# Kernel optimization log

Hardware: AMD Instinct MI355X
Metric: run time of the kernel (lower is better)

The kernel has to match this reference:

```python
import jax, jax.numpy as jnp
import numpy as np

B, T, C = 2, 2048, 1024
H = 16
D = C // H          # head_dim = 64
WIN = 256           # local window


def _rope(x):
    # x: [B, H, T, D]; rotate pairs (even, odd) with per-pair frequencies.
    t = x.shape[2]
    d = x.shape[-1] // 2
    theta = 10000.0 ** (-(jnp.arange(d, dtype=x.dtype) / d))          # [d]
    ang = jnp.arange(t, dtype=x.dtype)[:, None] * theta               # [T, d]
    sin, cos = jnp.sin(ang), jnp.cos(ang)                             # [T, d]
    x1, x2 = x[..., ::2], x[..., 1::2]                                # [B,H,T,d]
    out = jnp.stack([x1 * cos - x2 * sin, x1 * sin + x2 * cos], axis=-1)
    return out.reshape(x.shape)


def setup_inputs() -> dict:
    key = jax.random.key(0)
    k1, k2, k3 = jax.random.split(key, 3)
    s = 1.0 / np.sqrt(C)
    return {
        "x": jax.random.normal(k1, (B, T, C), dtype=jnp.float32),
        "w_qkv": jax.random.normal(k2, (3 * C, C), dtype=jnp.float32) * s,
        "w_out": jax.random.normal(k3, (C, C), dtype=jnp.float32) * s,
        "b_out": jnp.zeros((C,), dtype=jnp.float32),
    }


def reference(x, w_qkv, w_out, b_out):
    b, t, c = x.shape
    qkv = x @ w_qkv.T                                   # [B,T,3C]
    qkv = qkv.reshape(b, t, H, 3 * D).transpose(0, 2, 1, 3)  # [B,H,T,3D]
    q, k, v = jnp.split(qkv, 3, axis=-1)                # each [B,H,T,D]
    q, k = _rope(q), _rope(k)
    scores = jnp.einsum("bhqd,bhkd->bhqk", q, k) / jnp.sqrt(jnp.asarray(D, x.dtype))
    i = jnp.arange(t)[:, None]
    j = jnp.arange(t)[None, :]
    mask = (j <= i) & (j >= i - WIN)                    # causal local window
    scores = jnp.where(mask, scores, -jnp.inf)
    attn = jax.nn.softmax(scores, axis=-1)              # [B,H,T,T]
    out = jnp.einsum("bhqk,bhkd->bhqd", attn, v)        # [B,H,T,D]
    out = out.transpose(0, 2, 1, 3).reshape(b, t, c)    # [B,T,C]
    return out @ w_out.T + b_out
```

## Files before the change

kernel.cpp:

```cpp
#include <hip/hip_runtime.h>
#include <math.h>

#define BB 2
#define TT 2048
#define CC 1024
#define HH 16
#define DD 64
#define WINW 256

constexpr int MROWS  = BB * TT;
constexpr int NQKV   = 3 * CC;
constexpr int QKV_LD = 3 * CC;

typedef unsigned short ushort_t;
typedef __attribute__((ext_vector_type(8))) short  bf16x8;
typedef __attribute__((ext_vector_type(4))) float  f32x4;
typedef __attribute__((ext_vector_type(8))) unsigned short u16x8;

__device__ __forceinline__ float bf2f(ushort_t u) {
    return __uint_as_float(((unsigned int)u) << 16);
}
__device__ __forceinline__ ushort_t f2bf(float f) {
    unsigned int u = __float_as_uint(f);
    u += 0x7fffu + ((u >> 16) & 1u);
    return (ushort_t)(u >> 16);
}

__device__ __forceinline__ void async16(void* lds, const void* g) {
    __builtin_amdgcn_global_load_lds(
        (const __attribute__((address_space(1))) unsigned int*)g,
        (__attribute__((address_space(3))) unsigned int*)lds, 16, 0, 0);
}

#define ROPE_LN 0.2878231366242557f

constexpr int NX = MROWS * CC;
constexpr int NQ = NQKV * CC;
constexpr int NO = CC * CC;

__global__ __launch_bounds__(256)
void convert_all(const float* __restrict__ x, const float* __restrict__ wq,
                 const float* __restrict__ wo, ushort_t* __restrict__ xb,
                 ushort_t* __restrict__ wqb, ushort_t* __restrict__ wob) {
    int i = (blockIdx.x * 256 + threadIdx.x) * 4;
    const float* src;
    ushort_t* dst;
    if (i < NX)           { src = x  + i;             dst = xb  + i; }
    else if (i < NX + NQ) { src = wq + (i - NX);      dst = wqb + (i - NX); }
    else                  { src = wo + (i - NX - NQ); dst = wob + (i - NX - NQ); }
    float4 v = *(const float4*)src;
    ushort4 o;
    o.x = f2bf(v.x); o.y = f2bf(v.y); o.z = f2bf(v.z); o.w = f2bf(v.w);
    *(ushort4*)dst = o;
}

__global__ __launch_bounds__(512)
void gemm1_8phase(const ushort_t* __restrict__ A, const ushort_t* __restrict__ Bw,
                  ushort_t* __restrict__ Cc) {
    constexpr int K = 1024, N = 3072, NT = 16;
    __shared__ __align__(16) ushort_t As[2][2][256 * 32];
    __shared__ __align__(16) ushort_t Bs[2][2][256 * 32];

    const int tid  = threadIdx.x;
    const int lane = tid & 63;
    const int w    = tid >> 6;
    const int wm   = w >> 2;
    const int wn   = w & 3;
    const int fr   = lane & 15;
    const int fq   = lane >> 4;

    const int nbx = NQKV / 256;
    int flat = blockIdx.y * nbx + blockIdx.x;
    flat = (flat & 7) * 24 + (flat >> 3);
    const int bm = (flat / nbx) * 256;
    const int bn = (flat % nbx) * 256;

    const int sr  = tid >> 2;
    const int dcb = tid & 3;
    const int scb = dcb ^ ((sr >> 1) & 3);

    const int cbr = fq ^ ((fr >> 1) & 3);

    f32x4 acc[8][4];
#pragma unroll
    for (int m = 0; m < 8; ++m)
#pragma unroll
        for (int n = 0; n < 4; ++n)
            acc[m][n] = f32x4{0.f, 0.f, 0.f, 0.f};

#pragma unroll
    for (int p = 0; p < 4; ++p) {
        const int skh = p >> 1;
        const bool isB = p & 1;
        const ushort_t* G = isB ? Bw : A;
        const int br = isB ? bn : bm;
        ushort_t* L = isB ? &Bs[0][skh][0] : &As[0][skh][0];
#pragma unroll
        for (int hh = 0; hh < 2; ++hh)
            async16(&L[(hh * 128 + sr) * 32 + dcb * 8],
                    G + (size_t)(br + hh * 128 + sr) * K + skh * 32 + scb * 8);
    }

    for (int t = 0; t < NT; ++t) {
        const int d  = t & 1;
        const int tn = (t + 1) & (NT - 1);
        bf16x8 bfr[4];

#pragma unroll
        for (int ph = 0; ph < 4; ++ph) {
            const int kh = ph >> 1;
            const int mh = ph & 1;

            {
                const int skh = ph >> 1;
                const bool isB = ph & 1;
                const ushort_t* G = isB ? Bw : A;
                const int br = isB ? bn : bm;
                ushort_t* L = isB ? &Bs[d ^ 1][skh][0] : &As[d ^ 1][skh][0];
#pragma unroll
                for (int hh = 0; hh < 2; ++hh)
                    async16(&L[(hh * 128 + sr) * 32 + dcb * 8],
                            G + (size_t)(br + hh * 128 + sr) * K
                              + (size_t)tn * 64 + skh * 32 + scb * 8);
            }

            bf16x8 afr[4];
            if (mh == 1) {
#pragma unroll
                for (int i = 0; i < 4; ++i) {
                    const int ra = wm * 128 + (4 + i) * 16 + fr;
                    afr[i] = *(const bf16x8*)&As[d][kh][ra * 32 + cbr * 8];
                }
            } else {
                asm volatile("s_waitcnt vmcnt(6)" ::: "memory");
            }
            __builtin_amdgcn_s_barrier();

            if (mh == 0) {
#pragma unroll
                for (int n = 0; n < 4; ++n) {
                    const int rb = wn * 64 + n * 16 + fr;
                    bfr[n] = *(const bf16x8*)&Bs[d][kh][rb * 32 + cbr * 8];
                }
#pragma unroll
                for (int i = 0; i < 4; ++i) {
                    const int ra = wm * 128 + i * 16 + fr;
                    afr[i] = *(const bf16x8*)&As[d][kh][ra * 32 + cbr * 8];
                }
            }

            __builtin_amdgcn_s_setprio(1);
#pragma unroll
            for (int i = 0; i < 4; ++i)
#pragma unroll
                for (int n = 0; n < 4; ++n)
                    acc[mh * 4 + i][n] = __builtin_amdgcn_mfma_f32_16x16x32_bf16(
                        afr[i], bfr[n], acc[mh * 4 + i][n], 0, 0, 0);
            __builtin_amdgcn_s_setprio(0);
            __builtin_amdgcn_s_barrier();
        }
    }

#pragma unroll
    for (int m = 0; m < 8; ++m)
#pragma unroll
        for (int n = 0; n < 4; ++n)
#pragma unroll
            for (int j = 0; j < 4; ++j) {
                const int row = bm + wm * 128 + m * 16 + fq * 4 + j;
                const int col = bn + wn * 64 + n * 16 + fr;
                Cc[(size_t)row * N + col] = f2bf(acc[m][n][j]);
            }
}

template <bool BIAS, bool OUT_BF16>
__global__ __launch_bounds__(256)
void gemm_nt_mfma(const ushort_t* __restrict__ A, const ushort_t* __restrict__ Bw,
                  const float* __restrict__ bias, void* __restrict__ Cc,
                  int M, int N, int K) {
    __shared__ __align__(16) ushort_t As[128 * 32];
    __shared__ __align__(16) ushort_t Bs[128 * 32];

    const int tid  = threadIdx.x;
    const int lane = tid & 63;
    const int wv   = tid >> 6;
    const int wr   = wv >> 1;
    const int wc   = wv & 1;

    const int nbx = gridDim.x;
    const int nwg = nbx * gridDim.y;
    int flat = blockIdx.y * nbx + blockIdx.x;
    flat = (flat & 7) * (nwg >> 3) + (flat >> 3);
    const int bm = (flat / nbx) * 128;
    const int bn = (flat % nbx) * 128;

    const int srow = tid >> 2;
    const int scol = (tid & 3) * 8;

    const ushort_t* Ag = A + (size_t)(bm + srow) * K + scol;
    const ushort_t* Bg = Bw + (size_t)(bn + srow) * K + scol;

    f32x4 acc[4][4];
#pragma unroll
    for (int m = 0; m < 4; ++m)
#pragma unroll
        for (int n = 0; n < 4; ++n)
            acc[m][n] = f32x4{0.f, 0.f, 0.f, 0.f};

    const int fr = lane & 15;
    const int fq = lane >> 4;

    for (int k0 = 0; k0 < K; k0 += 32) {
        async16(&As[tid * 8],        Ag);
        async16(&As[2048 + tid * 8], Ag + (size_t)64 * K);
        async16(&Bs[tid * 8],        Bg);
        async16(&Bs[2048 + tid * 8], Bg + (size_t)64 * K);
        Ag += 32; Bg += 32;
        __syncthreads();

        bf16x8 af[4], bfv[4];
#pragma unroll
        for (int m = 0; m < 4; ++m)
            af[m] = *(const bf16x8*)&As[(wr * 64 + m * 16 + fr) * 32 + fq * 8];
#pragma unroll
        for (int n = 0; n < 4; ++n)
            bfv[n] = *(const bf16x8*)&Bs[(wc * 64 + n * 16 + fr) * 32 + fq * 8];
#pragma unroll
        for (int m = 0; m < 4; ++m)
#pragma unroll
            for (int n = 0; n < 4; ++n)
                acc[m][n] = __builtin_amdgcn_mfma_f32_16x16x32_bf16(
                    af[m], bfv[n], acc[m][n], 0, 0, 0);
        __syncthreads();
    }

#pragma unroll
    for (int m = 0; m < 4; ++m) {
#pragma unroll
        for (int n = 0; n < 4; ++n) {
            const int col = bn + wc * 64 + n * 16 + fr;
            const float bv = BIAS ? bias[col] : 0.0f;
#pragma unroll
            for (int j = 0; j < 4; ++j) {
                const int row = bm + wr * 64 + m * 16 + fq * 4 + j;
                float v = acc[m][n][j] + bv;
                if (OUT_BF16)
                    ((ushort_t*)Cc)[(size_t)row * N + col] = f2bf(v);
                else
                    ((float*)Cc)[(size_t)row * N + col] = v;
            }
        }
    }
}

#define MASKNEG (-1e30f)

__global__ __launch_bounds__(512)
void attn_mfma(const ushort_t* __restrict__ qkv, ushort_t* __restrict__ out) {
    __shared__ __align__(16) ushort_t Ks[2][64 * 64];
    __shared__ __align__(16) ushort_t Vlin[2][64 * 64];
    __shared__ __align__(16) ushort_t Vt[64 * 72];
    __shared__ __align__(16) ushort_t Ps[8][16 * 72];

    const int tid  = threadIdx.x;
    const int lane = tid & 63;
    const int w    = tid >> 6;
    const int fr   = lane & 15;
    const int fq   = lane >> 4;

    const int blk = blockIdx.x;
    const int qt  = blk & 15;
    const int h   = (blk >> 4) & 15;
    const int b   = blk >> 8;
    const int q0  = qt * 128;

    const ushort_t* base = qkv + (size_t)(b * TT) * QKV_LD + h * (3 * DD);

    const int srow = tid >> 3;
    const int cbs  = (tid & 7) ^ (srow & 7);

    float thK[4];
#pragma unroll
    for (int e = 0; e < 4; ++e)
        thK[e] = __expf(-ROPE_LN * (float)(cbs * 4 + e));

    bf16x8 qf0, qf1;
    {
        const int tq = q0 + w * 16 + fr;
        const ushort_t* qrow = base + (size_t)tq * QKV_LD;
        u16x8 r0 = *(const u16x8*)(qrow + fq * 8);
        u16x8 r1 = *(const u16x8*)(qrow + 32 + fq * 8);
        const float tf = (float)tq;
#pragma unroll
        for (int e = 0; e < 4; ++e) {
            float th0 = __expf(-ROPE_LN * (float)(fq * 4 + e));
            float a0 = tf * th0;
            float s0 = __sinf(a0), c0 = __cosf(a0);
            float x1 = bf2f(r0[2 * e]), x2 = bf2f(r0[2 * e + 1]);
            r0[2 * e]     = f2bf(x1 * c0 - x2 * s0);
            r0[2 * e + 1] = f2bf(x1 * s0 + x2 * c0);
            float th1 = __expf(-ROPE_LN * (float)(16 + fq * 4 + e));
            float a1 = tf * th1;
            float s1 = __sinf(a1), c1 = __cosf(a1);
            float y1 = bf2f(r1[2 * e]), y2 = bf2f(r1[2 * e + 1]);
            r1[2 * e]     = f2bf(y1 * c1 - y2 * s1);
            r1[2 * e + 1] = f2bf(y1 * s1 + y2 * c1);
        }
        qf0 = *(bf16x8*)&r0;
        qf1 = *(bf16x8*)&r1;
    }

    f32x4 oacc[4];
#pragma unroll
    for (int nd = 0; nd < 4; ++nd) oacc[nd] = f32x4{0.f, 0.f, 0.f, 0.f};
    float mj[4], lj[4];
#pragma unroll
    for (int j = 0; j < 4; ++j) { mj[j] = MASKNEG; lj[j] = 0.f; }

    const int kstart = (q0 >= WINW) ? (q0 - WINW) : 0;
    const int ntiles = (q0 + 128 - kstart) >> 6;
    const int qlo = q0 + w * 16;

    {
        const ushort_t* src = base + (size_t)(kstart + srow) * QKV_LD + DD + cbs * 8;
        u16x8 kv = *(const u16x8*)src;
        const float tf = (float)(kstart + srow);
#pragma unroll
        for (int e = 0; e < 4; ++e) {
            float a = tf * thK[e];
            float s = __sinf(a), c = __cosf(a);
            float x1 = bf2f(kv[2 * e]), x2 = bf2f(kv[2 * e + 1]);
            kv[2 * e]     = f2bf(x1 * c - x2 * s);
            kv[2 * e + 1] = f2bf(x1 * s + x2 * c);
        }
        *(u16x8*)&Ks[0][tid * 8] = kv;
        async16(&Vlin[0][tid * 8], src + DD);
    }
    __syncthreads();

    int cur = 0;
    for (int t = 0; t < ntiles; ++t) {
        const int kt0 = kstart + t * 64;
        const bool pf = (t + 1 < ntiles);
        const bool act = (kt0 <= qlo + 15) && (kt0 + 63 >= qlo - WINW);

        u16x8 kpre;
        if (pf) {
            const ushort_t* src =
                base + (size_t)(kt0 + 64 + srow) * QKV_LD + DD + cbs * 8;
            kpre = *(const u16x8*)src;
            async16(&Vlin[cur ^ 1][tid * 8], src + DD);
        }

        {
            u16x8 vv = *(const u16x8*)&Vlin[cur][lane * 64 + ((w ^ (lane & 7)) * 8)];
#pragma unroll
            for (int e = 0; e < 8; ++e)
                Vt[(w * 8 + e) * 72 + lane] = vv[e];
        }

        if (act) {
            f32x4 s[4];
#pragma unroll
            for (int n = 0; n < 4; ++n) {
                const int krow = n * 16 + fr;
                bf16x8 kb0 = *(const bf16x8*)&Ks[cur][krow * 64 + ((fq ^ (krow & 7)) * 8)];
                bf16x8 kb1 = *(const bf16x8*)&Ks[cur][krow * 64 + (((fq + 4) ^ (krow & 7)) * 8)];
                f32x4 z = f32x4{0.f, 0.f, 0.f, 0.f};
                z = __builtin_amdgcn_mfma_f32_16x16x32_bf16(qf0, kb0, z, 0, 0, 0);
                s[n] = __builtin_amdgcn_mfma_f32_16x16x32_bf16(qf1, kb1, z, 0, 0, 0);
            }

            float pmax[4];
#pragma unroll
            for (int j = 0; j < 4; ++j) pmax[j] = MASKNEG;
#pragma unroll
            for (int n = 0; n < 4; ++n) {
                const int key = kt0 + n * 16 + fr;
#pragma unroll
                for (int j = 0; j < 4; ++j) {
                    const int qi = qlo + fq * 4 + j;
                    const bool ok = (key <= qi) && (key >= qi - WINW);
                    float sv = ok ? s[n][j] * 0.125f : MASKNEG;
                    s[n][j] = sv;
                    pmax[j] = fmaxf(pmax[j], sv);
                }
            }
#pragma unroll
            for (int off = 1; off < 16; off <<= 1)
#pragma unroll
                for (int j = 0; j < 4; ++j)
                    pmax[j] = fmaxf(pmax[j], __shfl_xor(pmax[j], off));

            float tl[4] = {0.f, 0.f, 0.f, 0.f};
#pragma unroll
            for (int j = 0; j < 4; ++j) {
                float mnew = fmaxf(mj[j], pmax[j]);
                float alpha = (mnew <= -1e29f) ? 1.0f : __expf(mj[j] - mnew);
                mj[j] = mnew;
                lj[j] *= alpha;
#pragma unroll
                for (int nd = 0; nd < 4; ++nd) oacc[nd][j] *= alpha;
            }
#pragma unroll
            for (int n = 0; n < 4; ++n) {
#pragma unroll
                for (int j = 0; j < 4; ++j) {
                    float sv = s[n][j];
                    float p = (sv <= -1e29f) ? 0.f : __expf(sv - mj[j]);
                    tl[j] += p;
                    Ps[w][(fq * 4 + j) * 72 + n * 16 + fr] = f2bf(p);
                }
            }
#pragma unroll
            for (int off = 1; off < 16; off <<= 1)
#pragma unroll
                for (int j = 0; j < 4; ++j)
                    tl[j] += __shfl_xor(tl[j], off);
#pragma unroll
            for (int j = 0; j < 4; ++j) lj[j] += tl[j];
        }

        if (pf) {
            const float tf = (float)(kt0 + 64 + srow);
#pragma unroll
            for (int e = 0; e < 4; ++e) {
                float a = tf * thK[e];
                float s2 = __sinf(a), c2 = __cosf(a);
                float x1 = bf2f(kpre[2 * e]), x2 = bf2f(kpre[2 * e + 1]);
                kpre[2 * e]     = f2bf(x1 * c2 - x2 * s2);
                kpre[2 * e + 1] = f2bf(x1 * s2 + x2 * c2);
            }
            *(u16x8*)&Ks[cur ^ 1][tid * 8] = kpre;
        }

        __syncthreads();

        if (act) {
            bf16x8 pa0 = *(const bf16x8*)&Ps[w][fr * 72 + fq * 8];
            bf16x8 pa1 = *(const bf16x8*)&Ps[w][fr * 72 + 32 + fq * 8];
#pragma unroll
            for (int nd = 0; nd < 4; ++nd) {
                bf16x8 vb0 = *(const bf16x8*)&Vt[(nd * 16 + fr) * 72 + fq * 8];
                bf16x8 vb1 = *(const bf16x8*)&Vt[(nd * 16 + fr) * 72 + 32 + fq * 8];
                oacc[nd] = __builtin_amdgcn_mfma_f32_16x16x32_bf16(pa0, vb0, oacc[nd], 0, 0, 0);
                oacc[nd] = __builtin_amdgcn_mfma_f32_16x16x32_bf16(pa1, vb1, oacc[nd], 0, 0, 0);
            }
        }

        __syncthreads();
        cur ^= 1;
    }

#pragma unroll
    for (int nd = 0; nd < 4; ++nd) {
#pragma unroll
        for (int j = 0; j < 4; ++j) {
            const int qi = qlo + fq * 4 + j;
            out[(size_t)(b * TT + qi) * CC + h * DD + nd * 16 + fr] =
                f2bf(oacc[nd][j] / lj[j]);
        }
    }
}

extern "C" void kernel_launch(void* const* d_in, const int* in_sizes, int n_in,
                              void* d_out, int out_size, void* d_ws, size_t ws_size,
                              hipStream_t stream) {
    const float* x     = (const float*)d_in[0];
    const float* w_qkv = (const float*)d_in[1];
    const float* w_out = (const float*)d_in[2];
    const float* b_out = (const float*)d_in[3];
    float* out = (float*)d_out;

    ushort_t* qkv_b  = (ushort_t*)d_ws;
    ushort_t* attn_b = qkv_b  + (size_t)MROWS * NQKV;
    ushort_t* xb     = attn_b + (size_t)MROWS * CC;
    ushort_t* wqb    = xb     + (size_t)MROWS * CC;
    ushort_t* wob    = wqb    + (size_t)NQKV * CC;

    convert_all<<<(NX + NQ + NO) / 1024, 256, 0, stream>>>(
        x, w_qkv, w_out, xb, wqb, wob);

    gemm1_8phase<<<dim3(NQKV / 256, MROWS / 256), 512, 0, stream>>>(
        xb, wqb, qkv_b);

    attn_mfma<<<BB * HH * (TT / 128), 512, 0, stream>>>(qkv_b, attn_b);

    gemm_nt_mfma<true, false><<<dim3(CC / 128, MROWS / 128), 256, 0, stream>>>(
        attn_b, wob, b_out, out, MROWS, CC, CC);
}
```

Measured before the change: 112.2 us.

## Transpose V into double-buffered LDS from registers and drop a barrier

In the attention kernel, V rows are now loaded into registers alongside K and written transposed straight into a double-buffered Vt tile, with row stride 74. This removes the Vlin staging buffer, the per-iteration LDS-to-LDS transpose, and one __syncthreads per key tile. In the QKV GEMM, A-fragment loads are unified after the barrier behind a sched_barrier, and a final vmcnt(0) wait is added before the epilogue. The odd 74-element stride makes 16-byte LDS reads of Vt unaligned, which risks slower or incorrect accesses. The V global loads are now synchronous register loads rather than async copies.

New measurement: 104.0 us. 1.08x faster.

```diff
diff --git a/kernel.cpp b/kernel.cpp
--- a/kernel.cpp
+++ b/kernel.cpp
@@ -124,17 +124,10 @@
                               + (size_t)tn * 64 + skh * 32 + scb * 8);
             }
 
-            bf16x8 afr[4];
-            if (mh == 1) {
-#pragma unroll
-                for (int i = 0; i < 4; ++i) {
-                    const int ra = wm * 128 + (4 + i) * 16 + fr;
-                    afr[i] = *(const bf16x8*)&As[d][kh][ra * 32 + cbr * 8];
-                }
-            } else {
+            if (mh == 0)
                 asm volatile("s_waitcnt vmcnt(6)" ::: "memory");
-            }
             __builtin_amdgcn_s_barrier();
+            __builtin_amdgcn_sched_barrier(0);
 
             if (mh == 0) {
 #pragma unroll
@@ -142,11 +135,12 @@
                     const int rb = wn * 64 + n * 16 + fr;
                     bfr[n] = *(const bf16x8*)&Bs[d][kh][rb * 32 + cbr * 8];
                 }
-#pragma unroll
-                for (int i = 0; i < 4; ++i) {
-                    const int ra = wm * 128 + i * 16 + fr;
-                    afr[i] = *(const bf16x8*)&As[d][kh][ra * 32 + cbr * 8];
-                }
+            }
+            bf16x8 afr[4];
+#pragma unroll
+            for (int i = 0; i < 4; ++i) {
+                const int ra = wm * 128 + (mh * 4 + i) * 16 + fr;
+                afr[i] = *(const bf16x8*)&As[d][kh][ra * 32 + cbr * 8];
             }
 
             __builtin_amdgcn_s_setprio(1);
@@ -160,6 +154,8 @@
             __builtin_amdgcn_s_barrier();
         }
     }
+
+    asm volatile("s_waitcnt vmcnt(0)" ::: "memory");
 
 #pragma unroll
     for (int m = 0; m < 8; ++m)
@@ -258,8 +254,7 @@
 __global__ __launch_bounds__(512)
 void attn_mfma(const ushort_t* __restrict__ qkv, ushort_t* __restrict__ out) {
     __shared__ __align__(16) ushort_t Ks[2][64 * 64];
-    __shared__ __align__(16) ushort_t Vlin[2][64 * 64];
-    __shared__ __align__(16) ushort_t Vt[64 * 72];
+    __shared__ __align__(16) ushort_t Vt[2][64 * 74];
     __shared__ __align__(16) ushort_t Ps[8][16 * 72];
 
     const int tid  = threadIdx.x;
@@ -277,7 +272,8 @@
     const ushort_t* base = qkv + (size_t)(b * TT) * QKV_LD + h * (3 * DD);
 
     const int srow = tid >> 3;
-    const int cbs  = (tid & 7) ^ (srow & 7);
+    const int dcb  = tid & 7;
+    const int cbs  = dcb ^ (srow & 7);
 
     float thK[4];
 #pragma unroll
@@ -322,8 +318,9 @@
     const int qlo = q0 + w * 16;
 
     {
-        const ushort_t* src = base + (size_t)(kstart + srow) * QKV_LD + DD + cbs * 8;
-        u16x8 kv = *(const u16x8*)src;
+        const ushort_t* rowp = base + (size_t)(kstart + srow) * QKV_LD;
+        u16x8 kv = *(const u16x8*)(rowp + DD + cbs * 8);
+        u16x8 vv = *(const u16x8*)(rowp + 2 * DD + dcb * 8);
         const float tf = (float)(kstart + srow);
 #pragma unroll
         for (int e = 0; e < 4; ++e) {
@@ -334,7 +331,9 @@
             kv[2 * e + 1] = f2bf(x1 * s + x2 * c);
         }
         *(u16x8*)&Ks[0][tid * 8] = kv;
-        async16(&Vlin[0][tid * 8], src + DD);
+#pragma unroll
+        for (int e = 0; e < 8; ++e)
+            Vt[0][(dcb * 8 + e) * 74 + srow] = vv[e];
     }
     __syncthreads();
 
@@ -344,19 +343,11 @@
         const bool pf = (t + 1 < ntiles);
         const bool act = (kt0 <= qlo + 15) && (kt0 + 63 >= qlo - WINW);
 
-        u16x8 kpre;
+        u16x8 kpre, vpre;
         if (pf) {
-            const ushort_t* src =
-                base + (size_t)(kt0 + 64 + srow) * QKV_LD + DD + cbs * 8;
-            kpre = *(const u16x8*)src;
-            async16(&Vlin[cur ^ 1][tid * 8], src + DD);
-        }
-
-        {
-            u16x8 vv = *(const u16x8*)&Vlin[cur][lane * 64 + ((w ^ (lane & 7)) * 8)];
-#pragma unroll
-            for (int e = 0; e < 8; ++e)
-                Vt[(w * 8 + e) * 72 + lane] = vv[e];
+            const ushort_t* rowp = base + (size_t)(kt0 + 64 + srow) * QKV_LD;
+            kpre = *(const u16x8*)(rowp + DD + cbs * 8);
+            vpre = *(const u16x8*)(rowp + 2 * DD + dcb * 8);
         }
 
         if (act) {
@@ -432,17 +423,18 @@
                 kpre[2 * e + 1] = f2bf(x1 * s2 + x2 * c2);
             }
             *(u16x8*)&Ks[cur ^ 1][tid * 8] = kpre;
-        }
-
-        __syncthreads();
+#pragma unroll
+            for (int e = 0; e < 8; ++e)
+                Vt[cur ^ 1][(dcb * 8 + e) * 74 + srow] = vpre[e];
+        }
 
         if (act) {
             bf16x8 pa0 = *(const bf16x8*)&Ps[w][fr * 72 + fq * 8];
             bf16x8 pa1 = *(const bf16x8*)&Ps[w][fr * 72 + 32 + fq * 8];
 #pragma unroll
             for (int nd = 0; nd < 4; ++nd) {
-                bf16x8 vb0 = *(const bf16x8*)&Vt[(nd * 16 + fr) * 72 + fq * 8];
-                bf16x8 vb1 = *(const bf16x8*)&Vt[(nd * 16 + fr) * 72 + 32 + fq * 8];
+                bf16x8 vb0 = *(const bf16x8*)&Vt[cur][(nd * 16 + fr) * 74 + fq * 8];
+                bf16x8 vb1 = *(const bf16x8*)&Vt[cur][(nd * 16 + fr) * 74 + 32 + fq * 8];
                 oacc[nd] = __builtin_amdgcn_mfma_f32_16x16x32_bf16(pa0, vb0, oacc[nd], 0, 0, 0);
                 oacc[nd] = __builtin_amdgcn_mfma_f32_16x16x32_bf16(pa1, vb1, oacc[nd], 0, 0, 0);
             }
```
